# Performance work log

Hardware: AMD Instinct MI355X
Metric: run time of the kernel (lower is better)

The kernel has to match this reference:

```python
import jax, jax.numpy as jnp
import numpy as np

N_NODES = 50000
N_EDGES = 800000
D_IN = 64
D_OUT = 64


def setup_inputs() -> dict:
    key = jax.random.key(0)
    k1, k2, k3, k4 = jax.random.split(key, 4)
    x = jax.random.normal(k1, (N_NODES, D_IN), dtype=jnp.float32)
    src = jax.random.randint(k2, (N_EDGES,), 0, N_NODES, dtype=jnp.int64)
    dst = jax.random.randint(k3, (N_EDGES,), 0, N_NODES, dtype=jnp.int64)
    W = jax.random.normal(k4, (D_IN, D_OUT), dtype=jnp.float32) / np.sqrt(D_IN)
    b = jnp.zeros((D_OUT,), dtype=jnp.float32)
    return {"x": x, "src": src, "dst": dst, "W": W, "b": b}


def reference(x, src, dst, W, b):
    # DGL GraphConv, norm='both': out = D_in^{-1/2} A D_out^{-1/2} x W + b
    n = x.shape[0]
    ones = jnp.ones(src.shape[0], dtype=x.dtype)
    out_deg = jax.ops.segment_sum(ones, src, num_segments=n)  # out-degree of each node
    in_deg = jax.ops.segment_sum(ones, dst, num_segments=n)   # in-degree of each node
    norm_src = jax.lax.rsqrt(jnp.clip(out_deg, 1.0))          # [N]
    norm_dst = jax.lax.rsqrt(jnp.clip(in_deg, 1.0))           # [N]
    h = x * norm_src[:, None]                                 # [N, D_in]
    msg = jnp.take(h, src, axis=0)                            # [E, D_in] gather
    agg = jax.ops.segment_sum(msg, dst, num_segments=n)       # [N, D_in] scatter-add
    agg = agg * norm_dst[:, None]
    return agg @ W + b                                        # [N, D_out]
```

## Files before the change

kernel.cpp:

```cpp
#include <hip/hip_runtime.h>
#include <hip/hip_fp16.h>

#define N_NODES 50000
#define N_EDGES 800000
#define D 64

#define SLICES 100
#define I4S    2000
#define NI4    200000
#define NWORDS 12512

typedef float vfloat2 __attribute__((ext_vector_type(2)));

#define CTR_OFF    0
#define BASE_OFF   256
#define END_OFF    200320
#define SNORM_OFF  400384
#define DNORM_OFF  600448
#define SSRC_OFF   800512
#define OCC_OFF    4000768
#define PART_OFF   4800768
#define Y16_OFF    14810368

__global__ __launch_bounds__(256) void degree_occ_kernel(const int4* __restrict__ src4,
                                                         const int4* __restrict__ dst4,
                                                         unsigned int* __restrict__ partial,
                                                         uchar4* __restrict__ occ4,
                                                         int* __restrict__ ctr) {
    __shared__ unsigned int hist[NWORDS];
    int tid = threadIdx.x;
    if (blockIdx.x == 0 && tid == 0) *ctr = 0;
    uint4* h4 = (uint4*)hist;
    for (int i = tid; i < NWORDS / 4; i += 256) h4[i] = make_uint4(0, 0, 0, 0);
    __syncthreads();

    int role  = blockIdx.x & 1;
    int slice = blockIdx.x >> 1;
    int beg = slice * I4S, end = beg + I4S;
    if (role == 0) {
        for (int i = beg + tid; i < end; i += 256) {
            int4 v = src4[i];
            atomicAdd(&hist[v.x >> 2], 1u << ((v.x & 3) * 8));
            atomicAdd(&hist[v.y >> 2], 1u << ((v.y & 3) * 8));
            atomicAdd(&hist[v.z >> 2], 1u << ((v.z & 3) * 8));
            atomicAdd(&hist[v.w >> 2], 1u << ((v.w & 3) * 8));
        }
    } else {
        for (int i = beg + tid; i < end; i += 256) {
            int4 v = dst4[i];
            unsigned int o0 = (atomicAdd(&hist[v.x >> 2], 1u << ((v.x & 3) * 8)) >> ((v.x & 3) * 8)) & 0xFFu;
            unsigned int o1 = (atomicAdd(&hist[v.y >> 2], 1u << ((v.y & 3) * 8)) >> ((v.y & 3) * 8)) & 0xFFu;
            unsigned int o2 = (atomicAdd(&hist[v.z >> 2], 1u << ((v.z & 3) * 8)) >> ((v.z & 3) * 8)) & 0xFFu;
            unsigned int o3 = (atomicAdd(&hist[v.w >> 2], 1u << ((v.w & 3) * 8)) >> ((v.w & 3) * 8)) & 0xFFu;
            occ4[i] = make_uchar4((unsigned char)o0, (unsigned char)o1,
                                  (unsigned char)o2, (unsigned char)o3);
        }
    }
    __syncthreads();

    uint4* p4 = (uint4*)(partial + (size_t)blockIdx.x * NWORDS);
    for (int i = tid; i < NWORDS / 4; i += 256) p4[i] = h4[i];
}

__global__ __launch_bounds__(256) void merge_scan_kernel(unsigned int* __restrict__ partial,
                                                         int* __restrict__ base,
                                                         int* __restrict__ rend,
                                                         float* __restrict__ snorm,
                                                         float* __restrict__ dnorm,
                                                         int* __restrict__ ctr) {
    int w = blockIdx.x * blockDim.x + threadIdx.x;
    int lane = threadIdx.x & 63;
    unsigned int accin = 0, accout = 0;
    if (w < 12500) {
        unsigned int* po = partial + w;
        unsigned int* pd = partial + NWORDS + w;
#pragma unroll 4
        for (int s = 0; s < SLICES; s++) {
            size_t off = (size_t)(2 * s) * NWORDS;
            accout += po[off];
            unsigned int v = pd[off];
            pd[off] = accin;
            accin += v;
        }
    }
    int d0 = accin & 0xFF, d1 = (accin >> 8) & 0xFF,
        d2 = (accin >> 16) & 0xFF, d3 = (accin >> 24) & 0xFF;
    int tsum = d0 + d1 + d2 + d3;
    int run = tsum;
#pragma unroll
    for (int off = 1; off < 64; off <<= 1) {
        int v = __shfl_up(run, off);
        if (lane >= off) run += v;
    }
    int wtot = __shfl(run, 63);
    int wbase = 0;
    if (lane == 63) wbase = atomicAdd(ctr, wtot);
    wbase = __shfl(wbase, 63);
    if (w < 12500) {
        int b0 = wbase + run - tsum;
        int b1 = b0 + d0, b2 = b1 + d1, b3 = b2 + d2;
        ((int4*)base)[w] = make_int4(b0, b1, b2, b3);
        ((int4*)rend)[w] = make_int4(b1, b2, b3, b3 + d3);
        ((float4*)dnorm)[w] = make_float4(rsqrtf(fmaxf((float)d0, 1.f)),
                                          rsqrtf(fmaxf((float)d1, 1.f)),
                                          rsqrtf(fmaxf((float)d2, 1.f)),
                                          rsqrtf(fmaxf((float)d3, 1.f)));
        int o0 = accout & 0xFF, o1 = (accout >> 8) & 0xFF,
            o2 = (accout >> 16) & 0xFF, o3 = (accout >> 24) & 0xFF;
        ((float4*)snorm)[w] = make_float4(rsqrtf(fmaxf((float)o0, 1.f)),
                                          rsqrtf(fmaxf((float)o1, 1.f)),
                                          rsqrtf(fmaxf((float)o2, 1.f)),
                                          rsqrtf(fmaxf((float)o3, 1.f)));
    }
}

#define FYBLK 1024
__global__ __launch_bounds__(256, 4) void filly_kernel(const int4* __restrict__ src4,
                                                       const int4* __restrict__ dst4,
                                                       const uchar4* __restrict__ occ4,
                                                       const unsigned int* __restrict__ partial,
                                                       const int* __restrict__ base,
                                                       int* __restrict__ ssrc,
                                                       const float* __restrict__ x,
                                                       const float* __restrict__ snorm,
                                                       const float* __restrict__ W,
                                                       __half* __restrict__ y16) {
    int tid = blockIdx.x * blockDim.x + threadIdx.x;
    int lane = threadIdx.x & 63;

    if (tid < NI4) {
        int s = tid / I4S;
        const unsigned int* pref = partial + (size_t)(2 * s + 1) * NWORDS;
        int4 sv = src4[tid], tv = dst4[tid];
        uchar4 oc = occ4[tid];
#define FILL_ONE(T, S, O)                                                     \
        {                                                                     \
            int t = (T); int sh = (t & 3) * 8;                                \
            int p = base[t] + (int)((pref[t >> 2] >> sh) & 0xFFu) + (int)(O); \
            ssrc[p] = (S);                                                    \
        }
        FILL_ONE(tv.x, sv.x, oc.x)
        FILL_ONE(tv.y, sv.y, oc.y)
        FILL_ONE(tv.z, sv.z, oc.z)
        FILL_ONE(tv.w, sv.w, oc.w)
#undef FILL_ONE
    }

    float Wreg[D];
#pragma unroll
    for (int k = 0; k < D; k++) Wreg[k] = W[k * D + lane];
    int wave = tid >> 6;
    const int nwaves = FYBLK * 4;
    for (int n = wave; n < N_NODES; n += nwaves) {
        float hv = x[(size_t)n * D + lane] * snorm[n];
        int hb = __float_as_int(hv);
        float p0 = 0.f, p1 = 0.f, p2 = 0.f, p3 = 0.f;
#pragma unroll
        for (int k = 0; k < D; k += 4) {
            p0 = fmaf(__int_as_float(__builtin_amdgcn_readlane(hb, k + 0)), Wreg[k + 0], p0);
            p1 = fmaf(__int_as_float(__builtin_amdgcn_readlane(hb, k + 1)), Wreg[k + 1], p1);
            p2 = fmaf(__int_as_float(__builtin_amdgcn_readlane(hb, k + 2)), Wreg[k + 2], p2);
            p3 = fmaf(__int_as_float(__builtin_amdgcn_readlane(hb, k + 3)), Wreg[k + 3], p3);
        }
        y16[(size_t)n * D + lane] = __float2half((p0 + p1) + (p2 + p3));
    }
}

#define GBLK 2048
__global__ __launch_bounds__(256, 8) void gather_kernel(const __half2* __restrict__ y2,
                                                        const int* __restrict__ ssrc,
                                                        const int* __restrict__ base,
                                                        const int* __restrict__ rend,
                                                        const float* __restrict__ dnorm,
                                                        const float* __restrict__ b,
                                                        float* __restrict__ out) {
    int lane = threadIdx.x & 63;
    int half = lane & 1;
    int col  = lane >> 1;
    int wave = (blockIdx.x << 2) | (threadIdx.x >> 6);

    float2 b2 = ((const float2*)b)[col];
    const __half2* yl = y2 + col;

    for (int n = wave; n < N_NODES; n += GBLK * 4) {
        int beg = base[n], end = rend[n];
        float ax0 = 0.f, ay0 = 0.f, ax1 = 0.f, ay1 = 0.f;
        float ax2 = 0.f, ay2 = 0.f, ax3 = 0.f, ay3 = 0.f;
        float ax4 = 0.f, ay4 = 0.f, ax5 = 0.f, ay5 = 0.f;
        float ax6 = 0.f, ay6 = 0.f, ax7 = 0.f, ay7 = 0.f;
        int i0 = beg;
        for (; i0 + 16 <= end; i0 += 16) {
            int e = i0 + half;
            int s0 = ssrc[e],      s1 = ssrc[e + 2],  s2 = ssrc[e + 4],  s3 = ssrc[e + 6];
            int s4 = ssrc[e + 8],  s5 = ssrc[e + 10], s6 = ssrc[e + 12], s7 = ssrc[e + 14];
            float2 f0 = __half22float2(yl[(size_t)s0 * 32]);
            float2 f1 = __half22float2(yl[(size_t)s1 * 32]);
            float2 f2 = __half22float2(yl[(size_t)s2 * 32]);
            float2 f3 = __half22float2(yl[(size_t)s3 * 32]);
            float2 f4 = __half22float2(yl[(size_t)s4 * 32]);
            float2 f5 = __half22float2(yl[(size_t)s5 * 32]);
            float2 f6 = __half22float2(yl[(size_t)s6 * 32]);
            float2 f7 = __half22float2(yl[(size_t)s7 * 32]);
            ax0 += f0.x; ay0 += f0.y; ax1 += f1.x; ay1 += f1.y;
            ax2 += f2.x; ay2 += f2.y; ax3 += f3.x; ay3 += f3.y;
            ax4 += f4.x; ay4 += f4.y; ax5 += f5.x; ay5 += f5.y;
            ax6 += f6.x; ay6 += f6.y; ax7 += f7.x; ay7 += f7.y;
        }
        for (; i0 + 2 <= end; i0 += 2) {
            int s = ssrc[i0 + half];
            float2 f = __half22float2(yl[(size_t)s * 32]);
            ax0 += f.x; ay0 += f.y;
        }
        if (i0 < end && half == 0) {
            int s = ssrc[i0];
            float2 f = __half22float2(yl[(size_t)s * 32]);
            ax1 += f.x; ay1 += f.y;
        }
        float sx = ((ax0 + ax1) + (ax2 + ax3)) + ((ax4 + ax5) + (ax6 + ax7));
        float sy = ((ay0 + ay1) + (ay2 + ay3)) + ((ay4 + ay5) + (ay6 + ay7));
        sx += __shfl(sx, lane ^ 1);
        sy += __shfl(sy, lane ^ 1);
        if (half == 0) {
            float dn = dnorm[n];
            vfloat2 o;
            o.x = fmaf(sx, dn, b2.x);
            o.y = fmaf(sy, dn, b2.y);
            __builtin_nontemporal_store(o, (vfloat2*)(out + (size_t)n * D) + col);
        }
    }
}

extern "C" void kernel_launch(void* const* d_in, const int* in_sizes, int n_in,
                              void* d_out, int out_size, void* d_ws, size_t ws_size,
                              hipStream_t stream) {
    const float* x   = (const float*)d_in[0];
    const int*   src = (const int*)d_in[1];
    const int*   dst = (const int*)d_in[2];
    const float* W   = (const float*)d_in[3];
    const float* b   = (const float*)d_in[4];
    float* out = (float*)d_out;

    char* ws = (char*)d_ws;
    int*          ctr   = (int*)(ws + CTR_OFF);
    int*          base  = (int*)(ws + BASE_OFF);
    int*          rend  = (int*)(ws + END_OFF);
    float*        snorm = (float*)(ws + SNORM_OFF);
    float*        dnorm = (float*)(ws + DNORM_OFF);
    int*          ssrc  = (int*)(ws + SSRC_OFF);
    uchar4*       occ4  = (uchar4*)(ws + OCC_OFF);
    unsigned int* part  = (unsigned int*)(ws + PART_OFF);
    __half*       y16   = (__half*)(ws + Y16_OFF);

    const int4* src4 = (const int4*)src;
    const int4* dst4 = (const int4*)dst;

    degree_occ_kernel<<<2 * SLICES, 256, 0, stream>>>(src4, dst4, part, occ4, ctr);
    merge_scan_kernel<<<(12500 + 255) / 256, 256, 0, stream>>>(part, base, rend,
                                                               snorm, dnorm, ctr);
    filly_kernel<<<FYBLK, 256, 0, stream>>>(src4, dst4, occ4, part, base, ssrc,
                                            x, snorm, W, y16);
    gather_kernel<<<GBLK, 256, 0, stream>>>((const __half2*)y16, ssrc, base, rend,
                                            dnorm, b, out);
}
```

Measured before the change: 151.5 us.

## Split fp16 feature table into two column halves and gather per half

The transformed feature table is stored as two separate 32-column fp16 arrays instead of one 64-column array. The gather kernel splits its blocks into two passes, one per half. Each wave covers 4 edges at a time with 16 lanes per 64-byte row, then reduces across lane groups with shuffles. The intent is to shrink the working set each pass touches so the randomly gathered rows stay in cache. The cost is reading the index list twice and doing an extra shuffle reduction step.

```diff
diff --git a/kernel.cpp b/kernel.cpp
--- a/kernel.cpp
+++ b/kernel.cpp
@@ -20,7 +20,8 @@
 #define SSRC_OFF   800512
 #define OCC_OFF    4000768
 #define PART_OFF   4800768
-#define Y16_OFF    14810368
+#define YA_OFF     14810368
+#define YB_OFF     18010624
 
 __global__ __launch_bounds__(256) void degree_occ_kernel(const int4* __restrict__ src4,
                                                          const int4* __restrict__ dst4,
@@ -124,7 +125,8 @@
                                                        const float* __restrict__ x,
                                                        const float* __restrict__ snorm,
                                                        const float* __restrict__ W,
-                                                       __half* __restrict__ y16) {
+                                                       __half* __restrict__ yA,
+                                                       __half* __restrict__ yB) {
     int tid = blockIdx.x * blockDim.x + threadIdx.x;
     int lane = threadIdx.x & 63;
 
@@ -149,6 +151,8 @@
     float Wreg[D];
 #pragma unroll
     for (int k = 0; k < D; k++) Wreg[k] = W[k * D + lane];
+    __half* yh = (lane < 32) ? yA : yB;
+    int jl = lane & 31;
     int wave = tid >> 6;
     const int nwaves = FYBLK * 4;
     for (int n = wave; n < N_NODES; n += nwaves) {
@@ -162,72 +166,70 @@
             p2 = fmaf(__int_as_float(__builtin_amdgcn_readlane(hb, k + 2)), Wreg[k + 2], p2);
             p3 = fmaf(__int_as_float(__builtin_amdgcn_readlane(hb, k + 3)), Wreg[k + 3], p3);
         }
-        y16[(size_t)n * D + lane] = __float2half((p0 + p1) + (p2 + p3));
+        yh[(size_t)n * 32 + jl] = __float2half((p0 + p1) + (p2 + p3));
     }
 }
 
 #define GBLK 2048
-__global__ __launch_bounds__(256, 8) void gather_kernel(const __half2* __restrict__ y2,
+__global__ __launch_bounds__(256, 8) void gather_kernel(const __half2* __restrict__ yA,
+                                                        const __half2* __restrict__ yB,
                                                         const int* __restrict__ ssrc,
                                                         const int* __restrict__ base,
                                                         const int* __restrict__ rend,
                                                         const float* __restrict__ dnorm,
-                                                        const float* __restrict__ b,
+                                                        const float* __restrict__ bias,
                                                         float* __restrict__ out) {
     int lane = threadIdx.x & 63;
-    int half = lane & 1;
-    int col  = lane >> 1;
-    int wave = (blockIdx.x << 2) | (threadIdx.x >> 6);
-
-    float2 b2 = ((const float2*)b)[col];
-    const __half2* yl = y2 + col;
-
-    for (int n = wave; n < N_NODES; n += GBLK * 4) {
+    int q = lane >> 4;
+    int c = lane & 15;
+    int pass = blockIdx.x & 1;
+    int pblk = blockIdx.x >> 1;
+    int wave = (pblk << 2) | (threadIdx.x >> 6);
+    const int nwaves = (GBLK / 2) * 4;
+
+    float2 b2 = ((const float2*)bias)[(pass << 4) + c];
+    const __half2* ycol = (pass ? yB : yA) + c;
+
+#define ACC(A, F) { (A).x += (F).x; (A).y += (F).y; }
+
+    for (int n = wave; n < N_NODES; n += nwaves) {
         int beg = base[n], end = rend[n];
-        float ax0 = 0.f, ay0 = 0.f, ax1 = 0.f, ay1 = 0.f;
-        float ax2 = 0.f, ay2 = 0.f, ax3 = 0.f, ay3 = 0.f;
-        float ax4 = 0.f, ay4 = 0.f, ax5 = 0.f, ay5 = 0.f;
-        float ax6 = 0.f, ay6 = 0.f, ax7 = 0.f, ay7 = 0.f;
-        int i0 = beg;
-        for (; i0 + 16 <= end; i0 += 16) {
-            int e = i0 + half;
-            int s0 = ssrc[e],      s1 = ssrc[e + 2],  s2 = ssrc[e + 4],  s3 = ssrc[e + 6];
-            int s4 = ssrc[e + 8],  s5 = ssrc[e + 10], s6 = ssrc[e + 12], s7 = ssrc[e + 14];
-            float2 f0 = __half22float2(yl[(size_t)s0 * 32]);
-            float2 f1 = __half22float2(yl[(size_t)s1 * 32]);
-            float2 f2 = __half22float2(yl[(size_t)s2 * 32]);
-            float2 f3 = __half22float2(yl[(size_t)s3 * 32]);
-            float2 f4 = __half22float2(yl[(size_t)s4 * 32]);
-            float2 f5 = __half22float2(yl[(size_t)s5 * 32]);
-            float2 f6 = __half22float2(yl[(size_t)s6 * 32]);
-            float2 f7 = __half22float2(yl[(size_t)s7 * 32]);
-            ax0 += f0.x; ay0 += f0.y; ax1 += f1.x; ay1 += f1.y;
-            ax2 += f2.x; ay2 += f2.y; ax3 += f3.x; ay3 += f3.y;
-            ax4 += f4.x; ay4 += f4.y; ax5 += f5.x; ay5 += f5.y;
-            ax6 += f6.x; ay6 += f6.y; ax7 += f7.x; ay7 += f7.y;
-        }
-        for (; i0 + 2 <= end; i0 += 2) {
-            int s = ssrc[i0 + half];
-            float2 f = __half22float2(yl[(size_t)s * 32]);
-            ax0 += f.x; ay0 += f.y;
-        }
-        if (i0 < end && half == 0) {
-            int s = ssrc[i0];
-            float2 f = __half22float2(yl[(size_t)s * 32]);
-            ax1 += f.x; ay1 += f.y;
-        }
-        float sx = ((ax0 + ax1) + (ax2 + ax3)) + ((ax4 + ax5) + (ax6 + ax7));
-        float sy = ((ay0 + ay1) + (ay2 + ay3)) + ((ay4 + ay5) + (ay6 + ay7));
-        sx += __shfl(sx, lane ^ 1);
-        sy += __shfl(sy, lane ^ 1);
-        if (half == 0) {
-            float dn = dnorm[n];
+        float dn = dnorm[n];
+        float2 a0 = make_float2(0.f, 0.f), a1 = a0, a2 = a0, a3 = a0;
+        int i = beg;
+        for (; i + 16 <= end; i += 16) {
+            int s0 = ssrc[i + q],      s1 = ssrc[i + 4 + q];
+            int s2 = ssrc[i + 8 + q],  s3 = ssrc[i + 12 + q];
+            float2 f0 = __half22float2(ycol[(size_t)s0 * 16]);
+            float2 f1 = __half22float2(ycol[(size_t)s1 * 16]);
+            float2 f2 = __half22float2(ycol[(size_t)s2 * 16]);
+            float2 f3 = __half22float2(ycol[(size_t)s3 * 16]);
+            ACC(a0, f0) ACC(a1, f1) ACC(a2, f2) ACC(a3, f3)
+        }
+        for (; i + 4 <= end; i += 4) {
+            int s = ssrc[i + q];
+            float2 f = __half22float2(ycol[(size_t)s * 16]);
+            ACC(a0, f)
+        }
+        int rem = end - i;
+        if (q < rem) {
+            int s = ssrc[i + q];
+            float2 f = __half22float2(ycol[(size_t)s * 16]);
+            ACC(a1, f)
+        }
+        float2 t;
+        t.x = (a0.x + a1.x) + (a2.x + a3.x);
+        t.y = (a0.y + a1.y) + (a2.y + a3.y);
+        t.x += __shfl(t.x, lane ^ 16); t.y += __shfl(t.y, lane ^ 16);
+        t.x += __shfl(t.x, lane ^ 32); t.y += __shfl(t.y, lane ^ 32);
+        if (q == 0) {
             vfloat2 o;
-            o.x = fmaf(sx, dn, b2.x);
-            o.y = fmaf(sy, dn, b2.y);
-            __builtin_nontemporal_store(o, (vfloat2*)(out + (size_t)n * D) + col);
-        }
-    }
+            o.x = fmaf(t.x, dn, b2.x);
+            o.y = fmaf(t.y, dn, b2.y);
+            __builtin_nontemporal_store(o, (vfloat2*)(out + (size_t)n * D + (pass << 5)) + c);
+        }
+    }
+#undef ACC
 }
 
 extern "C" void kernel_launch(void* const* d_in, const int* in_sizes, int n_in,
@@ -249,7 +251,8 @@
     int*          ssrc  = (int*)(ws + SSRC_OFF);
     uchar4*       occ4  = (uchar4*)(ws + OCC_OFF);
     unsigned int* part  = (unsigned int*)(ws + PART_OFF);
-    __half*       y16   = (__half*)(ws + Y16_OFF);
+    __half*       yA    = (__half*)(ws + YA_OFF);
+    __half*       yB    = (__half*)(ws + YB_OFF);
 
     const int4* src4 = (const int4*)src;
     const int4* dst4 = (const int4*)dst;
@@ -258,7 +261,7 @@
     merge_scan_kernel<<<(12500 + 255) / 256, 256, 0, stream>>>(part, base, rend,
                                                                snorm, dnorm, ctr);
     filly_kernel<<<FYBLK, 256, 0, stream>>>(src4, dst4, occ4, part, base, ssrc,
-                                            x, snorm, W, y16);
-    gather_kernel<<<GBLK, 256, 0, stream>>>((const __half2*)y16, ssrc, base, rend,
-                                            dnorm, b, out);
-}
+                                            x, snorm, W, yA, yB);
+    gather_kernel<<<GBLK, 256, 0, stream>>>((const __half2*)yA, (const __half2*)yB,
+                                            ssrc, base, rend, dnorm, b, out);
+}
```

Measured after the change: 149.4 us, median of 2. No clear change (-1.3%).
